# Kernel optimization log

Measured on AMD Instinct MI355X. Metric: run time of the kernel, lower is better.

## Reference

```python
import jax, jax.numpy as jnp
import numpy as np

B, S, D = 4, 512, 256

def setup_inputs() -> dict:
    key = jax.random.key(0)
    ks = jax.random.split(key, 32)
    def w(k, shape, s=0.05):
        return jax.random.normal(k, shape, dtype=jnp.float32) * s
    inp = {
        "img": jax.random.normal(ks[0], (B, S, D), dtype=jnp.float32),
        "audio": jax.random.normal(ks[1], (B, S, D), dtype=jnp.float32),
        "common": jax.random.normal(ks[2], (B, S, D), dtype=jnp.float32),
    }
    names = ["qv", "qa", "kv", "ka", "cc", "w5", "w6", "w7", "w8"]
    for i, n in enumerate(names):
        inp[n + "_w"] = w(ks[3 + 2 * i], (D, D))   # stored [in, out]
        inp[n + "_b"] = w(ks[4 + 2 * i], (D,))
    inp["bil_w"] = w(ks[25], (D, D, D))            # Bilinear weight [out, in1, in2]
    inp["t_o"] = jnp.ones((), dtype=jnp.float32)
    return inp


def reference(img, audio, common,
              qv_w, qv_b, qa_w, qa_b, kv_w, kv_b, ka_w, ka_b, cc_w, cc_b,
              w5_w, w5_b, w6_w, w6_b, w7_w, w7_b, w8_w, w8_b,
              bil_w, t_o):
    dim_k = qv_w.shape[1]
    norm_fact = 1.0 / jnp.sqrt(jnp.asarray(dim_k, dtype=jnp.float32))

    lin = lambda x, w, b: x @ w + b
    # NOTE: faithful to source - softmax first, THEN scaled by norm_fact.
    attn = lambda q, k: jax.nn.softmax(jnp.einsum('bsd,btd->bst', q, k), axis=-1) * norm_fact

    W_q_v = lin(img, qv_w, qv_b)
    W_q_a = lin(audio, qa_w, qa_b)
    w_k_a = lin(audio, ka_w, ka_b)
    W_k_v = lin(img, kv_w, kv_b)
    C_c = lin(common, cc_w, cc_b)

    atten_vv = attn(W_q_v, W_k_v)
    atten_vc = attn(W_q_v, C_c)
    atten_aa = attn(W_q_a, w_k_a)
    atten_ac = attn(W_q_a, C_c)

    vc_common = jnp.einsum('bst,btd->bsd', atten_vc, common)
    ac_common = jnp.einsum('bst,btd->bsd', atten_ac, common)

    common_feat_v = (1.0 + lin(vc_common, w5_w, w5_b)) * jnp.einsum('bst,btd->bsd', atten_vv, img) + lin(vc_common, w6_w, w6_b)
    common_feat_a = (1.0 + lin(ac_common, w7_w, w7_b)) * jnp.einsum('bst,btd->bsd', atten_aa, audio) + lin(ac_common, w8_w, w8_b)

    # Bilinear: out[b,s,k] = v[b,s,:] @ W[k] @ a[b,s,:]
    atten_m = jnp.einsum('bsi,kij,bsj->bsk', common_feat_v, bil_w, common_feat_a)
    j_o = jax.nn.sigmoid(atten_m)
    Z_k_o = t_o * j_o * img + (1.0 - j_o) * audio
    return (Z_k_o + img, Z_k_o + audio)
```

## Files before the change

kernel.cpp:

```cpp
#include <hip/hip_runtime.h>
#include <hip/hip_bf16.h>

typedef unsigned short ushortT;
typedef __bf16 bf16x8 __attribute__((ext_vector_type(8)));
typedef float f32x4 __attribute__((ext_vector_type(4)));
typedef ushortT ush8 __attribute__((ext_vector_type(8)));
typedef ushortT ush4 __attribute__((ext_vector_type(4)));

#define MFMA16(a, b, c) __builtin_amdgcn_mfma_f32_16x16x32_bf16((a), (b), (c), 0, 0, 0)

__device__ __forceinline__ ushortT f2b(float f) {
  __hip_bfloat16 h = __float2bfloat16(f);
  return __builtin_bit_cast(ushortT, h);
}
__device__ __forceinline__ float b2f(ushortT u) {
  __hip_bfloat16 h = __builtin_bit_cast(__hip_bfloat16, u);
  return __bfloat162float(h);
}

__device__ __forceinline__ void async16(const void* g, void* l) {
  __builtin_amdgcn_global_load_lds((const __attribute__((address_space(1))) unsigned int*)g,
                                   (__attribute__((address_space(3))) unsigned int*)l, 16, 0, 0);
}

__device__ __forceinline__ bf16x8 scale8(bf16x8 a, float s) {
  union { bf16x8 v; unsigned int u[4]; } in, out;
  in.v = a;
#pragma unroll
  for (int p = 0; p < 4; p++) {
    float lo = __builtin_bit_cast(float, in.u[p] << 16);
    float hi = __builtin_bit_cast(float, in.u[p] & 0xffff0000u);
    lo *= s;
    hi *= s;
    unsigned int r;
    asm("v_cvt_pk_bf16_f32 %0, %1, %2" : "=v"(r) : "v"(lo), "v"(hi));
    out.u[p] = r;
  }
  return out.v;
}

#define ACT_E 524288
#define WD_E  65536

#define OFF_ACT16   0u
#define OFF_ACTT16  3145728u
#define OFF_W16T    6291456u
#define OFF_PROJ16  7471104u
#define OFF_P16     12713984u
#define OFF_VC16    21102592u
#define OFF_AC16    22151168u
#define OFF_PVV32   23199744u
#define OFF_PVA32   25296896u
#define OFF_PART    0u
#define OFF_BIL16   33554432u
#define OFF_CFV16   67108864u
#define OFF_CFA16   68157440u

__global__ void k_prep(const float* __restrict__ img, const float* __restrict__ aud,
                       const float* __restrict__ com,
                       const float* w0, const float* w1, const float* w2,
                       const float* w3, const float* w4, const float* w5,
                       const float* w6, const float* w7, const float* w8,
                       const float* __restrict__ bil,
                       ushortT* __restrict__ act16, ushortT* __restrict__ actT,
                       ushortT* __restrict__ wT, ushortT* __restrict__ bil16) {
  int tid = threadIdx.x;
  int bx = blockIdx.x;
  if (bx >= 528) {
    int i4 = (bx - 528) * 256 + tid;
#pragma unroll
    for (int q = 0; q < 8; q++) {
      int idx4 = i4 + q * 524288;
      float4 v = *(const float4*)(bil + (size_t)idx4 * 4);
      ush4 u = { f2b(v.x), f2b(v.y), f2b(v.z), f2b(v.w) };
      *(ush4*)(bil16 + (size_t)idx4 * 4) = u;
    }
    return;
  }
  __shared__ ushortT tl[64][72];
  const float* src;
  ushortT* dst;
  ushortT* lin = nullptr;
  int C, r0, c0, R;
  if (bx < 384) {
    int inst = bx >> 5, tile = bx & 31;
    int act = inst >> 2, bb = inst & 3;
    src = (act == 0 ? img : (act == 1 ? aud : com)) + bb * 131072;
    dst = actT + act * 524288 + bb * 131072;
    lin = act16 + act * 524288 + bb * 131072;
    R = 512; C = 256;
    r0 = (tile >> 2) * 64; c0 = (tile & 3) * 64;
  } else {
    int bw = bx - 384;
    int w = bw >> 4, tile = bw & 15;
    const float* s;
    switch (w) {
      case 0: s = w0; break; case 1: s = w1; break; case 2: s = w2; break;
      case 3: s = w3; break; case 4: s = w4; break; case 5: s = w5; break;
      case 6: s = w6; break; case 7: s = w7; break; default: s = w8; break;
    }
    src = s;
    dst = wT + w * 65536;
    R = 256; C = 256;
    r0 = (tile >> 2) * 64; c0 = (tile & 3) * 64;
  }
#pragma unroll
  for (int q = 0; q < 4; q++) {
    int rr = q * 16 + (tid >> 4);
    int cs = (tid & 15) * 4;
    float4 v = *(const float4*)(src + (r0 + rr) * C + c0 + cs);
    ush4 u = { f2b(v.x), f2b(v.y), f2b(v.z), f2b(v.w) };
    tl[rr][cs + 0] = u[0];
    tl[rr][cs + 1] = u[1];
    tl[rr][cs + 2] = u[2];
    tl[rr][cs + 3] = u[3];
    if (lin) *(ush4*)(lin + (r0 + rr) * 256 + c0 + cs) = u;
  }
  __syncthreads();
#pragma unroll
  for (int q = 0; q < 4; q++) {
    int cc = q * 16 + (tid >> 4);
    int rs = (tid & 15) * 4;
    ush4 u = { tl[rs + 0][cc], tl[rs + 1][cc], tl[rs + 2][cc], tl[rs + 3][cc] };
    *(ush4*)(dst + (c0 + cc) * R + r0 + rs) = u;
  }
}

__global__ __launch_bounds__(512) void k_linear5(
    const ushortT* __restrict__ act16, const ushortT* __restrict__ wT,
    const float* __restrict__ b0, const float* __restrict__ b1,
    const float* __restrict__ b2, const float* __restrict__ b3,
    const float* __restrict__ b4, ushortT* __restrict__ proj16) {
  __shared__ ushortT Al[4][32][8];
  __shared__ ushortT Bl[4][256][8];
  const int tid = threadIdx.x, l = tid & 63, w = tid >> 6;
  const int bx = blockIdx.x;
  const int op = bx >> 6, sblk = bx & 63;
  const int s0 = sblk * 32;
  const int xsel = (op == 4) ? 2 : (op & 1);
  const ushortT* X = act16 + xsel * ACT_E;
  const ushortT* W = wT + op * WD_E;
  const float* bias = op == 0 ? b0 : op == 1 ? b1 : op == 2 ? b2 : op == 3 ? b3 : b4;
  ushortT* out = proj16 + op * ACT_E;

  f32x4 acc[2][2] = {};
  ush8 ra, rb[2];
  int a_row = tid >> 2, a_seg = tid & 3;

  auto sload = [&](int k0) {
    if (tid < 128) ra = *(const ush8*)(X + (s0 + a_row) * 256 + k0 + a_seg * 8);
#pragma unroll
    for (int q = 0; q < 2; q++) {
      int slot = tid + q * 512;
      rb[q] = *(const ush8*)(W + (slot >> 2) * 256 + k0 + (slot & 3) * 8);
    }
  };
  auto swrite = [&]() {
    if (tid < 128) *(ush8*)(&Al[a_seg][a_row][0]) = ra;
#pragma unroll
    for (int q = 0; q < 2; q++) {
      int slot = tid + q * 512;
      *(ush8*)(&Bl[slot & 3][slot >> 2][0]) = rb[q];
    }
  };

  sload(0); swrite(); __syncthreads();
  for (int s = 0; s < 8; s++) {
    if (s < 7) sload((s + 1) * 32);
    int ks = l >> 4;
    bf16x8 a[2], bb[2];
#pragma unroll
    for (int m = 0; m < 2; m++) a[m] = *(const bf16x8*)(&Al[ks][m * 16 + (l & 15)][0]);
#pragma unroll
    for (int n = 0; n < 2; n++) bb[n] = *(const bf16x8*)(&Bl[ks][w * 32 + n * 16 + (l & 15)][0]);
#pragma unroll
    for (int m = 0; m < 2; m++)
#pragma unroll
      for (int n = 0; n < 2; n++) acc[m][n] = MFMA16(a[m], bb[n], acc[m][n]);
    if (s == 7) break;
    __syncthreads();
    swrite();
    __syncthreads();
  }
#pragma unroll
  for (int m = 0; m < 2; m++)
#pragma unroll
    for (int n = 0; n < 2; n++)
#pragma unroll
      for (int r = 0; r < 4; r++) {
        int row = s0 + m * 16 + (l >> 4) * 4 + r;
        int col = w * 32 + n * 16 + (l & 15);
        out[row * 256 + col] = f2b(acc[m][n][r] + bias[col]);
      }
}

__global__ __launch_bounds__(512) void k_attnpv(
    const ushortT* __restrict__ proj16, const ushortT* __restrict__ actT,
    float* __restrict__ pvv, float* __restrict__ pva,
    ushortT* __restrict__ vc16, ushortT* __restrict__ ac16) {
  __shared__ char arena[82944];
  auto Ql = (ushortT(*)[4][32][8])(arena);
  auto Kl = (ushortT(*)[512][8])(arena + 16384);
  auto Pl = (ushortT(*)[4][32][8])(arena + 49152);
  auto Vl = (ushortT(*)[256][8])(arena);
  auto red = (float(*)[8])(arena + 81920);

  const int tid = threadIdx.x, l = tid & 63, w = tid >> 6;
  const int bx = blockIdx.x;
  const int p = bx >> 6, b = (bx >> 4) & 3, sblk = bx & 15;
  const int s0 = sblk * 32;
  const int qsel = (p < 2) ? 0 : 1;
  const int ksel = (p == 0) ? 2 : (p == 2) ? 3 : 4;
  const int vsel = (p == 0) ? 0 : (p == 2) ? 1 : 2;
  const ushortT* Q = proj16 + qsel * ACT_E + b * 131072;
  const ushortT* K = proj16 + ksel * ACT_E + b * 131072;
  const ushortT* VT = actT + vsel * ACT_E + b * 131072;

#pragma unroll
  for (int q = 0; q < 2; q++) {
    int slot = tid + q * 512;
    int row = slot >> 5, seg = slot & 31;
    ush8 v = *(const ush8*)(Q + (s0 + row) * 256 + seg * 8);
    *(ush8*)(&Ql[seg >> 2][seg & 3][row][0]) = v;
  }

  f32x4 acc[2][4] = {};
  ush8 rk[4];
  auto kload = [&](int d0) {
#pragma unroll
    for (int q = 0; q < 4; q++) {
      int slot = tid + q * 512;
      rk[q] = *(const ush8*)(K + (slot >> 2) * 256 + d0 + (slot & 3) * 8);
    }
  };
  auto kwrite = [&]() {
#pragma unroll
    for (int q = 0; q < 4; q++) {
      int slot = tid + q * 512;
      *(ush8*)(&Kl[slot & 3][slot >> 2][0]) = rk[q];
    }
  };

  kload(0); kwrite(); __syncthreads();
  for (int s = 0; s < 8; s++) {
    if (s < 7) kload((s + 1) * 32);
    int ks = l >> 4;
    bf16x8 a[2], bb[4];
#pragma unroll
    for (int m = 0; m < 2; m++) a[m] = *(const bf16x8*)(&Ql[s][ks][m * 16 + (l & 15)][0]);
#pragma unroll
    for (int n = 0; n < 4; n++) bb[n] = *(const bf16x8*)(&Kl[ks][w * 64 + n * 16 + (l & 15)][0]);
#pragma unroll
    for (int m = 0; m < 2; m++)
#pragma unroll
      for (int n = 0; n < 4; n++) acc[m][n] = MFMA16(a[m], bb[n], acc[m][n]);
    if (s == 7) break;
    __syncthreads();
    kwrite();
    __syncthreads();
  }

  float gmax[2][4];
#pragma unroll
  for (int m = 0; m < 2; m++)
#pragma unroll
    for (int r = 0; r < 4; r++) {
      float v = fmaxf(fmaxf(acc[m][0][r], acc[m][1][r]), fmaxf(acc[m][2][r], acc[m][3][r]));
#pragma unroll
      for (int off = 1; off < 16; off <<= 1) v = fmaxf(v, __shfl_xor(v, off, 16));
      if ((l & 15) == 0) red[m * 16 + (l >> 4) * 4 + r][w] = v;
    }
  __syncthreads();
#pragma unroll
  for (int m = 0; m < 2; m++)
#pragma unroll
    for (int r = 0; r < 4; r++) {
      int sr = m * 16 + (l >> 4) * 4 + r;
      float g = red[sr][0];
#pragma unroll
      for (int ww = 1; ww < 8; ww++) g = fmaxf(g, red[sr][ww]);
      gmax[m][r] = g;
    }
  __syncthreads();
#pragma unroll
  for (int m = 0; m < 2; m++)
#pragma unroll
    for (int r = 0; r < 4; r++) {
      float ssum = 0.f;
#pragma unroll
      for (int n = 0; n < 4; n++) {
        float e = __expf(acc[m][n][r] - gmax[m][r]);
        acc[m][n][r] = e;
        ssum += e;
      }
#pragma unroll
      for (int off = 1; off < 16; off <<= 1) ssum += __shfl_xor(ssum, off, 16);
      if ((l & 15) == 0) red[m * 16 + (l >> 4) * 4 + r][w] = ssum;
    }
  __syncthreads();
#pragma unroll
  for (int m = 0; m < 2; m++)
#pragma unroll
    for (int r = 0; r < 4; r++) {
      int sr = m * 16 + (l >> 4) * 4 + r;
      float tot = 0.f;
#pragma unroll
      for (int ww = 0; ww < 8; ww++) tot += red[sr][ww];
      float sc = 0.0625f / tot;
#pragma unroll
      for (int n = 0; n < 4; n++) {
        int S = w * 2 + (n >> 1);
        int KS = ((n & 1) << 1) | ((l & 15) >> 3);
        Pl[S][KS][sr][l & 7] = f2b(acc[m][n][r] * sc);
      }
    }

  f32x4 acc2[2][2] = {};
  ush8 rv[2];
  auto vload = [&](int t0) {
#pragma unroll
    for (int q = 0; q < 2; q++) {
      int slot = tid + q * 512;
      rv[q] = *(const ush8*)(VT + (slot >> 2) * 512 + t0 + (slot & 3) * 8);
    }
  };
  auto vwrite = [&]() {
#pragma unroll
    for (int q = 0; q < 2; q++) {
      int slot = tid + q * 512;
      *(ush8*)(&Vl[slot & 3][slot >> 2][0]) = rv[q];
    }
  };

  vload(0);
  __syncthreads();
  vwrite();
  __syncthreads();
  for (int s = 0; s < 16; s++) {
    if (s < 15) vload((s + 1) * 32);
    int ks = l >> 4;
    bf16x8 a[2], bb[2];
#pragma unroll
    for (int m = 0; m < 2; m++) a[m] = *(const bf16x8*)(&Pl[s][ks][m * 16 + (l & 15)][0]);
#pragma unroll
    for (int n = 0; n < 2; n++) bb[n] = *(const bf16x8*)(&Vl[ks][w * 32 + n * 16 + (l & 15)][0]);
#pragma unroll
    for (int m = 0; m < 2; m++)
#pragma unroll
      for (int n = 0; n < 2; n++) acc2[m][n] = MFMA16(a[m], bb[n], acc2[m][n]);
    if (s == 15) break;
    __syncthreads();
    vwrite();
    __syncthreads();
  }
#pragma unroll
  for (int m = 0; m < 2; m++)
#pragma unroll
    for (int n = 0; n < 2; n++)
#pragma unroll
      for (int r = 0; r < 4; r++) {
        int row = s0 + m * 16 + (l >> 4) * 4 + r;
        int col = w * 32 + n * 16 + (l & 15);
        int gi = (b * 512 + row) * 256 + col;
        float v = acc2[m][n][r];
        if (p == 0) pvv[gi] = v;
        else if (p == 1) vc16[gi] = f2b(v);
        else if (p == 2) pva[gi] = v;
        else ac16[gi] = f2b(v);
      }
}

__global__ __launch_bounds__(512) void k_lin4c(
    const ushortT* __restrict__ vc16, const ushortT* __restrict__ ac16,
    const ushortT* __restrict__ wT,
    const float* __restrict__ w5b, const float* __restrict__ w6b,
    const float* __restrict__ w7b, const float* __restrict__ w8b,
    const float* __restrict__ pvv, const float* __restrict__ pva,
    ushortT* __restrict__ cfv, ushortT* __restrict__ cfa) {
  __shared__ ushortT Al[4][32][8];
  __shared__ ushortT B1[4][256][8];
  __shared__ ushortT B2[4][256][8];
  const int tid = threadIdx.x, l = tid & 63, w = tid >> 6;
  const int bx = blockIdx.x;
  const int side = bx >> 6, sblk = bx & 63;
  const int s0 = sblk * 32;
  const ushortT* A = side ? ac16 : vc16;
  const ushortT* W1 = wT + (side ? 7 : 5) * WD_E;
  const ushortT* W2 = wT + (side ? 8 : 6) * WD_E;
  const float* bb1 = side ? w7b : w5b;
  const float* bb2 = side ? w8b : w6b;
  const float* pv = side ? pva : pvv;
  ushortT* out = side ? cfa : cfv;

  f32x4 acc1[2][2] = {}, acc2[2][2] = {};
  ush8 ra, rb1[2], rb2[2];
  int a_row = tid >> 2, a_seg = tid & 3;
  auto sload = [&](int k0) {
    if (tid < 128) ra = *(const ush8*)(A + (s0 + a_row) * 256 + k0 + a_seg * 8);
#pragma unroll
    for (int q = 0; q < 2; q++) {
      int slot = tid + q * 512;
      rb1[q] = *(const ush8*)(W1 + (slot >> 2) * 256 + k0 + (slot & 3) * 8);
      rb2[q] = *(const ush8*)(W2 + (slot >> 2) * 256 + k0 + (slot & 3) * 8);
    }
  };
  auto swrite = [&]() {
    if (tid < 128) *(ush8*)(&Al[a_seg][a_row][0]) = ra;
#pragma unroll
    for (int q = 0; q < 2; q++) {
      int slot = tid + q * 512;
      *(ush8*)(&B1[slot & 3][slot >> 2][0]) = rb1[q];
      *(ush8*)(&B2[slot & 3][slot >> 2][0]) = rb2[q];
    }
  };

  sload(0); swrite(); __syncthreads();
  for (int s = 0; s < 8; s++) {
    if (s < 7) sload((s + 1) * 32);
    int ks = l >> 4;
    bf16x8 a[2], x1[2], x2[2];
#pragma unroll
    for (int m = 0; m < 2; m++) a[m] = *(const bf16x8*)(&Al[ks][m * 16 + (l & 15)][0]);
#pragma unroll
    for (int n = 0; n < 2; n++) {
      x1[n] = *(const bf16x8*)(&B1[ks][w * 32 + n * 16 + (l & 15)][0]);
      x2[n] = *(const bf16x8*)(&B2[ks][w * 32 + n * 16 + (l & 15)][0]);
    }
#pragma unroll
    for (int m = 0; m < 2; m++)
#pragma unroll
      for (int n = 0; n < 2; n++) {
        acc1[m][n] = MFMA16(a[m], x1[n], acc1[m][n]);
        acc2[m][n] = MFMA16(a[m], x2[n], acc2[m][n]);
      }
    if (s == 7) break;
    __syncthreads();
    swrite();
    __syncthreads();
  }
#pragma unroll
  for (int m = 0; m < 2; m++)
#pragma unroll
    for (int n = 0; n < 2; n++)
#pragma unroll
      for (int r = 0; r < 4; r++) {
        int row = s0 + m * 16 + (l >> 4) * 4 + r;
        int col = w * 32 + n * 16 + (l & 15);
        int gi = row * 256 + col;
        float u1 = acc1[m][n][r] + bb1[col];
        float u2 = acc2[m][n][r] + bb2[col];
        out[gi] = f2b((1.f + u1) * pv[gi] + u2);
      }
}

__global__ __launch_bounds__(512, 1) void k_bilinear8(
    const ushortT* __restrict__ cfa, const ushortT* __restrict__ cfv,
    const ushortT* __restrict__ W, ushortT* __restrict__ part) {
  __shared__ char arena[140288];
  const int tid = threadIdx.x, l = tid & 63, w = tid >> 6;
  const int d = blockIdx.x;
  const int L = (d & 7) * 32 + (d >> 3);
  const int ic = L >> 3;
  const int mb = L & 7;
  const int r0 = mb * 256;
  const int icb = ic * 8;
  const int wr = w >> 1, wc = w & 1;

  float* cfvl = (float*)(arena + 131072);
  if (tid < 256) {
    ush8 v = *(const ush8*)(cfv + (size_t)(r0 + tid) * 256 + icb);
    float* dp = cfvl + tid * 9;
#pragma unroll
    for (int q = 0; q < 8; q++) dp[q] = b2f(v[q]);
  }

  int pS[4], aOff[4], bOff[4], cvIdx[4];
#pragma unroll
  for (int s = 0; s < 4; s++) {
    int p = (tid + s * 512) * 16;
    int lg = p ^ (((p >> 7) & 7) << 4);
    int row = lg >> 7, colb = lg & 127;
    pS[s] = p;
    cvIdx[s] = row * 9;
    aOff[s] = (r0 + row) * 512 + colb;
    bOff[s] = row * 131072 + icb * 512 + colb;
  }
  const char* cfaB = (const char*)cfa;
  const char* WB = (const char*)W;

  int aoff[2][4], boff[2][8];
#pragma unroll
  for (int m = 0; m < 4; m++) {
    int row = wr * 64 + m * 16 + (l & 15);
    int b0 = row * 128 + (l >> 4) * 16;
    int msk = (row & 7) << 4;
    aoff[0][m] = b0 ^ msk;
    aoff[1][m] = (b0 + 64) ^ msk;
  }
#pragma unroll
  for (int n = 0; n < 8; n++) {
    int row = wc * 128 + n * 16 + (l & 15);
    int b0 = row * 128 + (l >> 4) * 16;
    int msk = (row & 7) << 4;
    boff[0][n] = b0 ^ msk;
    boff[1][n] = (b0 + 64) ^ msk;
  }

  ush8 arg[4];
  auto loadA = [&](int t) {
    int ja = (t & 3) << 7;
#pragma unroll
    for (int s = 0; s < 4; s++) arg[s] = *(const ush8*)(cfaB + aOff[s] + ja);
  };
  auto gloadB = [&](int t, char* Bb) {
    int jb = ((t >> 2) << 9) + ((t & 3) << 7);
#pragma unroll
    for (int s = 0; s < 4; s++) async16(WB + bOff[s] + jb, Bb + pS[s]);
  };
  auto writeA = [&](int t, char* Ab) {
    int ii = t >> 2;
#pragma unroll
    for (int s = 0; s < 4; s++) {
      float sc = cfvl[cvIdx[s] + ii];
      *(bf16x8*)(Ab + pS[s]) = scale8(__builtin_bit_cast(bf16x8, arg[s]), sc);
    }
  };

  f32x4 macc[4][8] = {};

  loadA(0);
  gloadB(0, arena + 65536);
  __syncthreads();
  writeA(0, arena);
  __syncthreads();

  for (int t = 0; t < 32; t++) {
    char* Ab = arena + ((t & 1) << 15);
    char* Bb = arena + 65536 + ((t & 1) << 15);
    char* An = arena + (((t + 1) & 1) << 15);
    char* Bn = arena + 65536 + (((t + 1) & 1) << 15);

    bf16x8 a0[4];
#pragma unroll
    for (int m = 0; m < 4; m++) a0[m] = *(const bf16x8*)(Ab + aoff[0][m]);

    if (t < 31) { loadA(t + 1); gloadB(t + 1, Bn); }

    {
      bf16x8 bl[4];
#pragma unroll
      for (int n = 0; n < 4; n++) bl[n] = *(const bf16x8*)(Bb + boff[0][n]);
      __builtin_amdgcn_s_setprio(1);
#pragma unroll
      for (int m = 0; m < 4; m++)
#pragma unroll
        for (int n = 0; n < 4; n++) macc[m][n] = MFMA16(a0[m], bl[n], macc[m][n]);
      __builtin_amdgcn_s_setprio(0);
    }
    {
      bf16x8 bh[4];
#pragma unroll
      for (int n = 0; n < 4; n++) bh[n] = *(const bf16x8*)(Bb + boff[0][n + 4]);
      __builtin_amdgcn_s_setprio(1);
#pragma unroll
      for (int m = 0; m < 4; m++)
#pragma unroll
        for (int n = 0; n < 4; n++) macc[m][n + 4] = MFMA16(a0[m], bh[n], macc[m][n + 4]);
      __builtin_amdgcn_s_setprio(0);
    }

    if (t < 31) writeA(t + 1, An);

    bf16x8 a1[4];
#pragma unroll
    for (int m = 0; m < 4; m++) a1[m] = *(const bf16x8*)(Ab + aoff[1][m]);
    {
      bf16x8 bl[4];
#pragma unroll
      for (int n = 0; n < 4; n++) bl[n] = *(const bf16x8*)(Bb + boff[1][n]);
      __builtin_amdgcn_s_setprio(1);
#pragma unroll
      for (int m = 0; m < 4; m++)
#pragma unroll
        for (int n = 0; n < 4; n++) macc[m][n] = MFMA16(a1[m], bl[n], macc[m][n]);
      __builtin_amdgcn_s_setprio(0);
    }
    {
      bf16x8 bh[4];
#pragma unroll
      for (int n = 0; n < 4; n++) bh[n] = *(const bf16x8*)(Bb + boff[1][n + 4]);
      __builtin_amdgcn_s_setprio(1);
#pragma unroll
      for (int m = 0; m < 4; m++)
#pragma unroll
        for (int n = 0; n < 4; n++) macc[m][n + 4] = MFMA16(a1[m], bh[n], macc[m][n + 4]);
      __builtin_amdgcn_s_setprio(0);
    }

    __syncthreads();
  }

  ushortT* dst = part + (size_t)ic * 524288 + (size_t)r0 * 256;
#pragma unroll
  for (int m = 0; m < 4; m++)
#pragma unroll
    for (int n = 0; n < 8; n++)
#pragma unroll
      for (int r = 0; r < 4; r++)
        dst[(wr * 64 + m * 16 + ((l >> 4) << 2) + r) * 256 + wc * 128 + n * 16 + (l & 15)] =
            f2b(macc[m][n][r]);
}

__global__ void k_final2(const ushortT* __restrict__ part, const float* __restrict__ img,
                         const float* __restrict__ aud, const float* __restrict__ t_o,
                         float* __restrict__ out0, float* __restrict__ out1) {
  int i = blockIdx.x * 256 + threadIdx.x;
  float t = t_o[0];
  float4 m = {0.f, 0.f, 0.f, 0.f};
#pragma unroll
  for (int ic = 0; ic < 32; ic++) {
    ush4 p = *(const ush4*)(part + (size_t)ic * 524288 + (size_t)i * 4);
    m.x += b2f(p[0]); m.y += b2f(p[1]); m.z += b2f(p[2]); m.w += b2f(p[3]);
  }
  float4 a = ((const float4*)img)[i];
  float4 u = ((const float4*)aud)[i];
  float4 o0, o1;
  {
    float j = 1.f / (1.f + __expf(-m.x)); float Z = t * j * a.x + (1.f - j) * u.x;
    o0.x = Z + a.x; o1.x = Z + u.x;
  }
  {
    float j = 1.f / (1.f + __expf(-m.y)); float Z = t * j * a.y + (1.f - j) * u.y;
    o0.y = Z + a.y; o1.y = Z + u.y;
  }
  {
    float j = 1.f / (1.f + __expf(-m.z)); float Z = t * j * a.z + (1.f - j) * u.z;
    o0.z = Z + a.z; o1.z = Z + u.z;
  }
  {
    float j = 1.f / (1.f + __expf(-m.w)); float Z = t * j * a.w + (1.f - j) * u.w;
    o0.w = Z + a.w; o1.w = Z + u.w;
  }
  ((float4*)out0)[i] = o0;
  ((float4*)out1)[i] = o1;
}

extern "C" void kernel_launch(void* const* d_in, const int* in_sizes, int n_in,
                              void* d_out, int out_size, void* d_ws, size_t ws_size,
                              hipStream_t stream) {
  const float* img   = (const float*)d_in[0];
  const float* aud   = (const float*)d_in[1];
  const float* com   = (const float*)d_in[2];
  const float* qv_w  = (const float*)d_in[3];
  const float* qv_b  = (const float*)d_in[4];
  const float* qa_w  = (const float*)d_in[5];
  const float* qa_b  = (const float*)d_in[6];
  const float* kv_w  = (const float*)d_in[7];
  const float* kv_b  = (const float*)d_in[8];
  const float* ka_w  = (const float*)d_in[9];
  const float* ka_b  = (const float*)d_in[10];
  const float* cc_w  = (const float*)d_in[11];
  const float* cc_b  = (const float*)d_in[12];
  const float* w5_w  = (const float*)d_in[13];
  const float* w5_b  = (const float*)d_in[14];
  const float* w6_w  = (const float*)d_in[15];
  const float* w6_b  = (const float*)d_in[16];
  const float* w7_w  = (const float*)d_in[17];
  const float* w7_b  = (const float*)d_in[18];
  const float* w8_w  = (const float*)d_in[19];
  const float* w8_b  = (const float*)d_in[20];
  const float* bil_w = (const float*)d_in[21];
  const float* t_o   = (const float*)d_in[22];
  float* out = (float*)d_out;

  char* ws = (char*)d_ws;
  ushortT* act16  = (ushortT*)(ws + OFF_ACT16);
  ushortT* actT16 = (ushortT*)(ws + OFF_ACTT16);
  ushortT* w16t   = (ushortT*)(ws + OFF_W16T);
  ushortT* proj16 = (ushortT*)(ws + OFF_PROJ16);
  ushortT* vc16   = (ushortT*)(ws + OFF_VC16);
  ushortT* ac16   = (ushortT*)(ws + OFF_AC16);
  float*   pvv32  = (float*)(ws + OFF_PVV32);
  float*   pva32  = (float*)(ws + OFF_PVA32);
  ushortT* part   = (ushortT*)(ws + OFF_PART);
  ushortT* bil16  = (ushortT*)(ws + OFF_BIL16);
  ushortT* cfv16  = (ushortT*)(ws + OFF_CFV16);
  ushortT* cfa16  = (ushortT*)(ws + OFF_CFA16);

  k_prep<<<2576, 256, 0, stream>>>(img, aud, com, qv_w, qa_w, kv_w, ka_w, cc_w,
                                   w5_w, w6_w, w7_w, w8_w, bil_w,
                                   act16, actT16, w16t, bil16);
  k_linear5<<<320, 512, 0, stream>>>(act16, w16t, qv_b, qa_b, kv_b, ka_b, cc_b, proj16);
  k_attnpv<<<256, 512, 0, stream>>>(proj16, actT16, pvv32, pva32, vc16, ac16);
  k_lin4c<<<128, 512, 0, stream>>>(vc16, ac16, w16t, w5_b, w6_b, w7_b, w8_b,
                                   pvv32, pva32, cfv16, cfa16);
  k_bilinear8<<<256, 512, 0, stream>>>(cfa16, cfv16, bil16, part);
  k_final2<<<512, 256, 0, stream>>>(part, img, aud, t_o, out, out + 524288);
}
```

Measured before the change: 137.1 us.

## Restructure bilinear main loop into four barrier-phased MFMA stages with interleaved loads

Rewrites the k_bilinear kernel's K-loop into four phases. Each phase loads a slice of B fragments from LDS, issues one piece of the next-tile global or LDS traffic (loadA, gloadB, writeA), then syncs with s_barrier and explicit waitcnt before running its MFMA cluster. This aims to overlap memory traffic with matrix work in a ping-pong style and keep waves in lockstep. In exchange it adds many more workgroup barriers per iteration and holds both A fragments live at once, which raises register pressure.

```diff
diff --git a/kernel.cpp b/kernel.cpp
--- a/kernel.cpp
+++ b/kernel.cpp
@@ -453,7 +453,7 @@
       }
 }
 
-__global__ __launch_bounds__(512, 1) void k_bilinear8(
+__global__ __launch_bounds__(512, 1) void k_bilinear9(
     const ushortT* __restrict__ cfa, const ushortT* __restrict__ cfv,
     const ushortT* __restrict__ W, ushortT* __restrict__ part) {
   __shared__ char arena[140288];
@@ -539,65 +539,91 @@
     char* Bb = arena + 65536 + ((t & 1) << 15);
     char* An = arena + (((t + 1) & 1) << 15);
     char* Bn = arena + 65536 + (((t + 1) & 1) << 15);
-
-    bf16x8 a0[4];
-#pragma unroll
-    for (int m = 0; m < 4; m++) a0[m] = *(const bf16x8*)(Ab + aoff[0][m]);
-
-    if (t < 31) { loadA(t + 1); gloadB(t + 1, Bn); }
-
-    {
-      bf16x8 bl[4];
-#pragma unroll
-      for (int n = 0; n < 4; n++) bl[n] = *(const bf16x8*)(Bb + boff[0][n]);
-      __builtin_amdgcn_s_setprio(1);
-#pragma unroll
-      for (int m = 0; m < 4; m++)
-#pragma unroll
-        for (int n = 0; n < 4; n++) macc[m][n] = MFMA16(a0[m], bl[n], macc[m][n]);
-      __builtin_amdgcn_s_setprio(0);
-    }
-    {
-      bf16x8 bh[4];
-#pragma unroll
-      for (int n = 0; n < 4; n++) bh[n] = *(const bf16x8*)(Bb + boff[0][n + 4]);
-      __builtin_amdgcn_s_setprio(1);
-#pragma unroll
-      for (int m = 0; m < 4; m++)
-#pragma unroll
-        for (int n = 0; n < 4; n++) macc[m][n + 4] = MFMA16(a0[m], bh[n], macc[m][n + 4]);
-      __builtin_amdgcn_s_setprio(0);
-    }
-
-    if (t < 31) writeA(t + 1, An);
-
-    bf16x8 a1[4];
-#pragma unroll
-    for (int m = 0; m < 4; m++) a1[m] = *(const bf16x8*)(Ab + aoff[1][m]);
-    {
-      bf16x8 bl[4];
-#pragma unroll
-      for (int n = 0; n < 4; n++) bl[n] = *(const bf16x8*)(Bb + boff[1][n]);
-      __builtin_amdgcn_s_setprio(1);
-#pragma unroll
-      for (int m = 0; m < 4; m++)
-#pragma unroll
-        for (int n = 0; n < 4; n++) macc[m][n] = MFMA16(a1[m], bl[n], macc[m][n]);
-      __builtin_amdgcn_s_setprio(0);
-    }
-    {
-      bf16x8 bh[4];
-#pragma unroll
-      for (int n = 0; n < 4; n++) bh[n] = *(const bf16x8*)(Bb + boff[1][n + 4]);
-      __builtin_amdgcn_s_setprio(1);
-#pragma unroll
-      for (int m = 0; m < 4; m++)
-#pragma unroll
-        for (int n = 0; n < 4; n++) macc[m][n + 4] = MFMA16(a1[m], bh[n], macc[m][n + 4]);
-      __builtin_amdgcn_s_setprio(0);
-    }
-
-    __syncthreads();
+    const bool more = (t < 31);
+
+    bf16x8 a0[4], a1[4], p0[2], p1[2];
+
+#pragma unroll
+    for (int m = 0; m < 4; m++) {
+      a0[m] = *(const bf16x8*)(Ab + aoff[0][m]);
+      a1[m] = *(const bf16x8*)(Ab + aoff[1][m]);
+    }
+    p0[0] = *(const bf16x8*)(Bb + boff[0][0]);
+    p0[1] = *(const bf16x8*)(Bb + boff[0][1]);
+    p1[0] = *(const bf16x8*)(Bb + boff[1][0]);
+    p1[1] = *(const bf16x8*)(Bb + boff[1][1]);
+    if (more) loadA(t + 1);
+    __builtin_amdgcn_s_barrier();
+    asm volatile("s_waitcnt lgkmcnt(0)" ::: "memory");
+    __builtin_amdgcn_sched_barrier(0);
+    __builtin_amdgcn_s_setprio(1);
+#pragma unroll
+    for (int m = 0; m < 4; m++) {
+      macc[m][0] = MFMA16(a0[m], p0[0], macc[m][0]);
+      macc[m][1] = MFMA16(a0[m], p0[1], macc[m][1]);
+      macc[m][0] = MFMA16(a1[m], p1[0], macc[m][0]);
+      macc[m][1] = MFMA16(a1[m], p1[1], macc[m][1]);
+    }
+    __builtin_amdgcn_s_setprio(0);
+    __builtin_amdgcn_s_barrier();
+
+    p0[0] = *(const bf16x8*)(Bb + boff[0][2]);
+    p0[1] = *(const bf16x8*)(Bb + boff[0][3]);
+    p1[0] = *(const bf16x8*)(Bb + boff[1][2]);
+    p1[1] = *(const bf16x8*)(Bb + boff[1][3]);
+    if (more) gloadB(t + 1, Bn);
+    __builtin_amdgcn_s_barrier();
+    asm volatile("s_waitcnt lgkmcnt(0)" ::: "memory");
+    __builtin_amdgcn_sched_barrier(0);
+    __builtin_amdgcn_s_setprio(1);
+#pragma unroll
+    for (int m = 0; m < 4; m++) {
+      macc[m][2] = MFMA16(a0[m], p0[0], macc[m][2]);
+      macc[m][3] = MFMA16(a0[m], p0[1], macc[m][3]);
+      macc[m][2] = MFMA16(a1[m], p1[0], macc[m][2]);
+      macc[m][3] = MFMA16(a1[m], p1[1], macc[m][3]);
+    }
+    __builtin_amdgcn_s_setprio(0);
+    __builtin_amdgcn_s_barrier();
+
+    p0[0] = *(const bf16x8*)(Bb + boff[0][4]);
+    p0[1] = *(const bf16x8*)(Bb + boff[0][5]);
+    p1[0] = *(const bf16x8*)(Bb + boff[1][4]);
+    p1[1] = *(const bf16x8*)(Bb + boff[1][5]);
+    if (more) writeA(t + 1, An);
+    __builtin_amdgcn_s_barrier();
+    asm volatile("s_waitcnt lgkmcnt(0)" ::: "memory");
+    __builtin_amdgcn_sched_barrier(0);
+    __builtin_amdgcn_s_setprio(1);
+#pragma unroll
+    for (int m = 0; m < 4; m++) {
+      macc[m][4] = MFMA16(a0[m], p0[0], macc[m][4]);
+      macc[m][5] = MFMA16(a0[m], p0[1], macc[m][5]);
+      macc[m][4] = MFMA16(a1[m], p1[0], macc[m][4]);
+      macc[m][5] = MFMA16(a1[m], p1[1], macc[m][5]);
+    }
+    __builtin_amdgcn_s_setprio(0);
+    __builtin_amdgcn_s_barrier();
+
+    p0[0] = *(const bf16x8*)(Bb + boff[0][6]);
+    p0[1] = *(const bf16x8*)(Bb + boff[0][7]);
+    p1[0] = *(const bf16x8*)(Bb + boff[1][6]);
+    p1[1] = *(const bf16x8*)(Bb + boff[1][7]);
+    __builtin_amdgcn_s_barrier();
+    asm volatile("s_waitcnt lgkmcnt(0)" ::: "memory");
+    __builtin_amdgcn_sched_barrier(0);
+    __builtin_amdgcn_s_setprio(1);
+#pragma unroll
+    for (int m = 0; m < 4; m++) {
+      macc[m][6] = MFMA16(a0[m], p0[0], macc[m][6]);
+      macc[m][7] = MFMA16(a0[m], p0[1], macc[m][7]);
+      macc[m][6] = MFMA16(a1[m], p1[0], macc[m][6]);
+      macc[m][7] = MFMA16(a1[m], p1[1], macc[m][7]);
+    }
+    __builtin_amdgcn_s_setprio(0);
+    asm volatile("s_waitcnt vmcnt(0)" ::: "memory");
+    __builtin_amdgcn_sched_barrier(0);
+    __builtin_amdgcn_s_barrier();
   }
 
   ushortT* dst = part + (size_t)ic * 524288 + (size_t)r0 * 256;
@@ -694,6 +720,6 @@
   k_attnpv<<<256, 512, 0, stream>>>(proj16, actT16, pvv32, pva32, vc16, ac16);
   k_lin4c<<<128, 512, 0, stream>>>(vc16, ac16, w16t, w5_b, w6_b, w7_b, w8_b,
                                    pvv32, pva32, cfv16, cfa16);
-  k_bilinear8<<<256, 512, 0, stream>>>(cfa16, cfv16, bil16, part);
+  k_bilinear9<<<256, 512, 0, stream>>>(cfa16, cfv16, bil16, part);
   k_final2<<<512, 256, 0, stream>>>(part, img, aud, t_o, out, out + 524288);
 }
```

After: 144.9 us. 1.06x slower.

## Keep bilinear A operand in registers and scale per step instead of staging in LDS

Applied to the files above, without the earlier changes.

The bilinear kernel no longer writes the cfv-scaled cfa tile into shared memory each step. Each wave now loads its cfa fragments straight from global into registers, reloading them once every eight k-steps. The B loop order is permuted so the j-chunk stays fixed while the i index cycles, and the scaling by cfv is applied in registers. This removes LDS write traffic, one barrier and half the LDS footprint, at the cost of more registers and redundant global reads of A across waves.

```diff
diff --git a/kernel.cpp b/kernel.cpp
--- a/kernel.cpp
+++ b/kernel.cpp
@@ -453,10 +453,10 @@
       }
 }
 
-__global__ __launch_bounds__(512, 1) void k_bilinear8(
+__global__ __launch_bounds__(512, 1) void k_bilinear10(
     const ushortT* __restrict__ cfa, const ushortT* __restrict__ cfv,
     const ushortT* __restrict__ W, ushortT* __restrict__ part) {
-  __shared__ char arena[140288];
+  __shared__ char arena[74752];
   const int tid = threadIdx.x, l = tid & 63, w = tid >> 6;
   const int d = blockIdx.x;
   const int L = (d & 7) * 32 + (d >> 3);
@@ -466,7 +466,7 @@
   const int icb = ic * 8;
   const int wr = w >> 1, wc = w & 1;
 
-  float* cfvl = (float*)(arena + 131072);
+  float* cfvl = (float*)(arena + 65536);
   if (tid < 256) {
     ush8 v = *(const ush8*)(cfv + (size_t)(r0 + tid) * 256 + icb);
     float* dp = cfvl + tid * 9;
@@ -474,29 +474,18 @@
     for (int q = 0; q < 8; q++) dp[q] = b2f(v[q]);
   }
 
-  int pS[4], aOff[4], bOff[4], cvIdx[4];
+  int pS[4], bOff[4];
 #pragma unroll
   for (int s = 0; s < 4; s++) {
     int p = (tid + s * 512) * 16;
     int lg = p ^ (((p >> 7) & 7) << 4);
     int row = lg >> 7, colb = lg & 127;
     pS[s] = p;
-    cvIdx[s] = row * 9;
-    aOff[s] = (r0 + row) * 512 + colb;
     bOff[s] = row * 131072 + icb * 512 + colb;
   }
-  const char* cfaB = (const char*)cfa;
   const char* WB = (const char*)W;
 
-  int aoff[2][4], boff[2][8];
-#pragma unroll
-  for (int m = 0; m < 4; m++) {
-    int row = wr * 64 + m * 16 + (l & 15);
-    int b0 = row * 128 + (l >> 4) * 16;
-    int msk = (row & 7) << 4;
-    aoff[0][m] = b0 ^ msk;
-    aoff[1][m] = (b0 + 64) ^ msk;
-  }
+  int boff[2][8];
 #pragma unroll
   for (int n = 0; n < 8; n++) {
     int row = wc * 128 + n * 16 + (l & 15);
@@ -506,96 +495,84 @@
     boff[1][n] = (b0 + 64) ^ msk;
   }
 
-  ush8 arg[4];
-  auto loadA = [&](int t) {
-    int ja = (t & 3) << 7;
-#pragma unroll
-    for (int s = 0; s < 4; s++) arg[s] = *(const ush8*)(cfaB + aOff[s] + ja);
+  const ushortT* gAbase = cfa + (size_t)(r0 + wr * 64 + (l & 15)) * 256 + (l >> 4) * 8;
+  const float* cfvp = cfvl + (wr * 64 + (l & 15)) * 9;
+
+  ush8 abase[8];
+  auto loadAjs = [&](int js) {
+#pragma unroll
+    for (int kc = 0; kc < 2; kc++)
+#pragma unroll
+      for (int m = 0; m < 4; m++)
+        abase[kc * 4 + m] = *(const ush8*)(gAbase + m * 4096 + kc * 32 + js * 64);
   };
   auto gloadB = [&](int t, char* Bb) {
-    int jb = ((t >> 2) << 9) + ((t & 3) << 7);
+    int jb = ((t & 7) << 9) + ((t >> 3) << 7);
 #pragma unroll
     for (int s = 0; s < 4; s++) async16(WB + bOff[s] + jb, Bb + pS[s]);
   };
-  auto writeA = [&](int t, char* Ab) {
-    int ii = t >> 2;
-#pragma unroll
-    for (int s = 0; s < 4; s++) {
-      float sc = cfvl[cvIdx[s] + ii];
-      *(bf16x8*)(Ab + pS[s]) = scale8(__builtin_bit_cast(bf16x8, arg[s]), sc);
-    }
-  };
 
   f32x4 macc[4][8] = {};
 
-  loadA(0);
-  gloadB(0, arena + 65536);
+  loadAjs(0);
+  gloadB(0, arena);
   __syncthreads();
-  writeA(0, arena);
-  __syncthreads();
 
   for (int t = 0; t < 32; t++) {
-    char* Ab = arena + ((t & 1) << 15);
-    char* Bb = arena + 65536 + ((t & 1) << 15);
-    char* An = arena + (((t + 1) & 1) << 15);
-    char* Bn = arena + 65536 + (((t + 1) & 1) << 15);
-
-    bf16x8 a0[4];
-#pragma unroll
-    for (int m = 0; m < 4; m++) a0[m] = *(const bf16x8*)(Ab + aoff[0][m]);
-
-    if (t < 31) { loadA(t + 1); gloadB(t + 1, Bn); }
-
-    {
-      bf16x8 bl[4];
-#pragma unroll
-      for (int n = 0; n < 4; n++) bl[n] = *(const bf16x8*)(Bb + boff[0][n]);
-      __builtin_amdgcn_s_setprio(1);
+    char* Bb = arena + ((t & 1) << 15);
+    char* Bn = arena + (((t + 1) & 1) << 15);
+    const int i = t & 7;
+
+    bf16x8 bf0[4], bf1[4];
+#pragma unroll
+    for (int n = 0; n < 4; n++) bf0[n] = *(const bf16x8*)(Bb + boff[0][n]);
+
+    float sc[4];
+#pragma unroll
+    for (int m = 0; m < 4; m++) sc[m] = cfvp[m * 144 + i];
+    bf16x8 aS[8];
+#pragma unroll
+    for (int kc = 0; kc < 2; kc++)
 #pragma unroll
       for (int m = 0; m < 4; m++)
-#pragma unroll
-        for (int n = 0; n < 4; n++) macc[m][n] = MFMA16(a0[m], bl[n], macc[m][n]);
-      __builtin_amdgcn_s_setprio(0);
-    }
-    {
-      bf16x8 bh[4];
-#pragma unroll
-      for (int n = 0; n < 4; n++) bh[n] = *(const bf16x8*)(Bb + boff[0][n + 4]);
-      __builtin_amdgcn_s_setprio(1);
-#pragma unroll
-      for (int m = 0; m < 4; m++)
-#pragma unroll
-        for (int n = 0; n < 4; n++) macc[m][n + 4] = MFMA16(a0[m], bh[n], macc[m][n + 4]);
-      __builtin_amdgcn_s_setprio(0);
-    }
-
-    if (t < 31) writeA(t + 1, An);
-
-    bf16x8 a1[4];
-#pragma unroll
-    for (int m = 0; m < 4; m++) a1[m] = *(const bf16x8*)(Ab + aoff[1][m]);
-    {
-      bf16x8 bl[4];
-#pragma unroll
-      for (int n = 0; n < 4; n++) bl[n] = *(const bf16x8*)(Bb + boff[1][n]);
-      __builtin_amdgcn_s_setprio(1);
-#pragma unroll
-      for (int m = 0; m < 4; m++)
-#pragma unroll
-        for (int n = 0; n < 4; n++) macc[m][n] = MFMA16(a1[m], bl[n], macc[m][n]);
-      __builtin_amdgcn_s_setprio(0);
-    }
-    {
-      bf16x8 bh[4];
-#pragma unroll
-      for (int n = 0; n < 4; n++) bh[n] = *(const bf16x8*)(Bb + boff[1][n + 4]);
-      __builtin_amdgcn_s_setprio(1);
-#pragma unroll
-      for (int m = 0; m < 4; m++)
-#pragma unroll
-        for (int n = 0; n < 4; n++) macc[m][n + 4] = MFMA16(a1[m], bh[n], macc[m][n + 4]);
-      __builtin_amdgcn_s_setprio(0);
-    }
+        aS[kc * 4 + m] = scale8(__builtin_bit_cast(bf16x8, abase[kc * 4 + m]), sc[m]);
+
+    if (t < 31) gloadB(t + 1, Bn);
+    if (i == 7 && t < 31) loadAjs((t >> 3) + 1);
+
+#pragma unroll
+    for (int n = 0; n < 4; n++) bf1[n] = *(const bf16x8*)(Bb + boff[0][n + 4]);
+    __builtin_amdgcn_s_setprio(1);
+#pragma unroll
+    for (int m = 0; m < 4; m++)
+#pragma unroll
+      for (int n = 0; n < 4; n++) macc[m][n] = MFMA16(aS[m], bf0[n], macc[m][n]);
+    __builtin_amdgcn_s_setprio(0);
+
+#pragma unroll
+    for (int n = 0; n < 4; n++) bf0[n] = *(const bf16x8*)(Bb + boff[1][n]);
+    __builtin_amdgcn_s_setprio(1);
+#pragma unroll
+    for (int m = 0; m < 4; m++)
+#pragma unroll
+      for (int n = 0; n < 4; n++) macc[m][n + 4] = MFMA16(aS[m], bf1[n], macc[m][n + 4]);
+    __builtin_amdgcn_s_setprio(0);
+
+#pragma unroll
+    for (int n = 0; n < 4; n++) bf1[n] = *(const bf16x8*)(Bb + boff[1][n + 4]);
+    __builtin_amdgcn_s_setprio(1);
+#pragma unroll
+    for (int m = 0; m < 4; m++)
+#pragma unroll
+      for (int n = 0; n < 4; n++) macc[m][n] = MFMA16(aS[4 + m], bf0[n], macc[m][n]);
+    __builtin_amdgcn_s_setprio(0);
+
+    __builtin_amdgcn_s_setprio(1);
+#pragma unroll
+    for (int m = 0; m < 4; m++)
+#pragma unroll
+      for (int n = 0; n < 4; n++) macc[m][n + 4] = MFMA16(aS[4 + m], bf1[n], macc[m][n + 4]);
+    __builtin_amdgcn_s_setprio(0);
 
     __syncthreads();
   }
@@ -694,6 +671,6 @@
   k_attnpv<<<256, 512, 0, stream>>>(proj16, actT16, pvv32, pva32, vc16, ac16);
   k_lin4c<<<128, 512, 0, stream>>>(vc16, ac16, w16t, w5_b, w6_b, w7_b, w8_b,
                                    pvv32, pva32, cfv16, cfa16);
-  k_bilinear8<<<256, 512, 0, stream>>>(cfa16, cfv16, bil16, part);
+  k_bilinear10<<<256, 512, 0, stream>>>(cfa16, cfv16, bil16, part);
   k_final2<<<512, 256, 0, stream>>>(part, img, aud, t_o, out, out + 524288);
 }
```

New measurement: 137.5 us. No clear change (+0.3%).
